# Performance work log

Hardware: AMD Instinct MI355X
Metric: run time of the kernel (lower is better)

## Reference

```python
import jax, jax.numpy as jnp
import numpy as np
from jax import lax

SEQ, BATCH, IN, HID, OUT = 168, 4096, 24, 64, 9


def _uniform(key, shape, scale):
    return jax.random.uniform(key, shape, jnp.float32, -scale, scale)


def setup_inputs() -> dict:
    key = jax.random.key(0)
    ks = jax.random.split(key, 12)
    s = 1.0 / np.sqrt(HID)  # PyTorch LSTM/Linear init scale
    return {
        "x": jax.random.normal(ks[0], (SEQ, BATCH, IN), jnp.float32),
        # layer 0 LSTM (PyTorch gate order: i, f, g, o stacked along dim 0)
        "W_ih0": _uniform(ks[1], (4 * HID, IN), s),
        "W_hh0": _uniform(ks[2], (4 * HID, HID), s),
        "b_ih0": _uniform(ks[3], (4 * HID,), s),
        "b_hh0": _uniform(ks[4], (4 * HID,), s),
        # layer 1 LSTM
        "W_ih1": _uniform(ks[5], (4 * HID, HID), s),
        "W_hh1": _uniform(ks[6], (4 * HID, HID), s),
        "b_ih1": _uniform(ks[7], (4 * HID,), s),
        "b_hh1": _uniform(ks[8], (4 * HID,), s),
        # linear head
        "W_out": _uniform(ks[9], (OUT, HID), s),
        "b_out": _uniform(ks[10], (OUT,), s),
    }


def _lstm_layer(x, W_ih, W_hh, b_ih, b_hh):
    # x: [S, B, D]; returns hidden states [S, B, H]
    H = W_hh.shape[1]
    B = x.shape[1]
    # precompute input projections for all timesteps: [S, B, 4H]
    xg = jnp.einsum('sbd,gd->sbg', x, W_ih) + b_ih + b_hh

    def step(carry, xg_t):
        h, c = carry
        g = xg_t + h @ W_hh.T  # [B, 4H]
        i, f, gc, o = jnp.split(g, 4, axis=-1)
        c = jax.nn.sigmoid(f) * c + jax.nn.sigmoid(i) * jnp.tanh(gc)
        h = jax.nn.sigmoid(o) * jnp.tanh(c)
        return (h, c), h

    init = (jnp.zeros((B, H), x.dtype), jnp.zeros((B, H), x.dtype))
    _, hs = lax.scan(step, init, xg)
    return hs


def reference(x, W_ih0, W_hh0, b_ih0, b_hh0, W_ih1, W_hh1, b_ih1, b_hh1, W_out, b_out):
    h = _lstm_layer(x, W_ih0, W_hh0, b_ih0, b_hh0)   # [S, B, H]
    h = _lstm_layer(h, W_ih1, W_hh1, b_ih1, b_hh1)   # [S, B, H]
    out = jnp.einsum('sbh,oh->sbo', h, W_out) + b_out  # [S, B, OUT]
    return out
```

## Files before the change

kernel.cpp:

```cpp
#include <hip/hip_runtime.h>
#include <hip/hip_bf16.h>
#include <math.h>

#define SEQ   168
#define BATCH 4096
#define NOUT  9
#define NBLK  256

typedef short bf16x8 __attribute__((ext_vector_type(8)));
typedef float f32x4  __attribute__((ext_vector_type(4)));

#define MFMA(a,b,c) __builtin_amdgcn_mfma_f32_16x16x32_bf16((a),(b),(c),0,0,0)

static __device__ __forceinline__ float bf2f(unsigned short h){
    unsigned int u = ((unsigned int)h) << 16;
    return __builtin_bit_cast(float, u);
}
static __device__ __forceinline__ unsigned short f2bf(float f){
    return __builtin_bit_cast(unsigned short, __float2bfloat16(f));
}
static __device__ __forceinline__ void splitf(float f, unsigned short& hi, unsigned short& lo){
    hi = f2bf(f);
    float r = f - bf2f(hi);
    lo = (unsigned short)(__builtin_bit_cast(unsigned int, r) >> 16);
}
static __device__ __forceinline__ float sigf(float x){
    return __builtin_amdgcn_rcpf(1.0f + __expf(-x));
}
static __device__ __forceinline__ float tanhf_(float x){
    float r = __builtin_amdgcn_rcpf(1.0f + __expf(2.0f * x));
    return fmaf(-2.0f, r, 1.0f);
}
static __device__ __forceinline__ bf16x8 ldfrag(const unsigned short* p){
    const uint4 q = *reinterpret_cast<const uint4*>(p);
    return __builtin_bit_cast(bf16x8, q);
}

static __device__ __forceinline__ void gbar(int* cnt, int* phs, int* done,
                                            int tickval, int& ph, int lane){
    asm volatile("s_waitcnt lgkmcnt(0)" ::: "memory");
    if (lane == 0){
        int old = __hip_atomic_fetch_add(cnt, 1, __ATOMIC_ACQ_REL,
                                         __HIP_MEMORY_SCOPE_WORKGROUP);
        if (old == 3){
            *cnt = 0;
            __hip_atomic_store(done, tickval, __ATOMIC_RELEASE,
                               __HIP_MEMORY_SCOPE_WORKGROUP);
            __hip_atomic_store(phs, ph ^ 1, __ATOMIC_RELEASE,
                               __HIP_MEMORY_SCOPE_WORKGROUP);
        }
    }
    while (__hip_atomic_load(phs, __ATOMIC_ACQUIRE,
                             __HIP_MEMORY_SCOPE_WORKGROUP) == ph)
        __builtin_amdgcn_s_sleep(1);
    ph ^= 1;
}
static __device__ __forceinline__ void wait_ge(int* done, int need){
    if (__hip_atomic_load(done, __ATOMIC_ACQUIRE, __HIP_MEMORY_SCOPE_WORKGROUP) >= need) return;
    do { __builtin_amdgcn_s_sleep(1); }
    while (__hip_atomic_load(done, __ATOMIC_ACQUIRE, __HIP_MEMORY_SCOPE_WORKGROUP) < need);
}

__global__ __launch_bounds__(512, 2)
void lstm_fused(const float* __restrict__ x,
                const float* __restrict__ Wih0, const float* __restrict__ Whh0,
                const float* __restrict__ bih0, const float* __restrict__ bhh0,
                const float* __restrict__ Wih1, const float* __restrict__ Whh1,
                const float* __restrict__ bih1, const float* __restrict__ bhh1,
                const float* __restrict__ Wout, const float* __restrict__ bout,
                float* __restrict__ out)
{
    __shared__ __align__(16) unsigned short sXH[2][16][72];
    __shared__ __align__(16) unsigned short sH0H[3][16][72];
    __shared__ __align__(16) unsigned short sH1H[2][16][72];
    __shared__ int sync[8];

    const int tid  = threadIdx.x;
    const int half = tid >> 8;
    const int w2   = (tid >> 6) & 3;
    const int l    = tid & 63;
    const int lr   = l & 15;
    const int g    = l >> 4;
    const int r0   = blockIdx.x * 16;
    const int cg   = w2 * 16 + lr;

    if (tid < 8) sync[tid] = (tid == 4) ? -1 : 0;

    for (int i = tid; i < (int)(2*16*72/2); i += 512){
        ((unsigned int*)sXH)[i]  = 0u;
        ((unsigned int*)sH1H)[i] = 0u;
    }
    for (int i = tid; i < (int)(3*16*72/2); i += 512)
        ((unsigned int*)sH0H)[i] = 0u;
    __syncthreads();
    if (tid < 96){
        const float4 v = *reinterpret_cast<const float4*>(&x[(size_t)r0 * 24 + tid * 4]);
        const int row = (tid * 4) / 24, col = (tid * 4) % 24;
        ushort4 w = { f2bf(v.x), f2bf(v.y), f2bf(v.z), f2bf(v.w) };
        *reinterpret_cast<ushort4*>(&sXH[0][row][col]) = w;
    }
    __syncthreads();

    if (half == 0){
        bf16x8 B0H[4][3];
        #pragma unroll
        for (int gt = 0; gt < 4; ++gt){
            const int c = gt * 64 + cg;
            bf16x8 bh = {0,0,0,0,0,0,0,0};
            if (g < 3){
                const float* pw = &Wih0[c * 24 + g * 8];
                #pragma unroll
                for (int j = 0; j < 8; ++j) bh[j] = (short)f2bf(pw[j]);
            }
            B0H[gt][0] = bh;
            #pragma unroll
            for (int ks = 0; ks < 2; ++ks){
                bf16x8 ch;
                const float* pw = &Whh0[c * 64 + ks * 32 + g * 8];
                #pragma unroll
                for (int j = 0; j < 8; ++j) ch[j] = (short)f2bf(pw[j]);
                B0H[gt][1+ks] = ch;
            }
        }
        float b0[4];
        #pragma unroll
        for (int gt = 0; gt < 4; ++gt) b0[gt] = bih0[gt*64 + cg] + bhh0[gt*64 + cg];

        const float* xfp = x + ((size_t)BATCH + r0) * 24 + tid * 4;
        float c0[4] = {0,0,0,0};
        int ph = 0;
        int pw = 0, pr = 2;
        for (int t = 0; t < SEQ; ++t){
            const int px = t & 1;
            const bool ldx = (tid < 96) && (t + 1 < SEQ);
            float4 pref;
            if (ldx){ pref = *reinterpret_cast<const float4*>(xfp); xfp += (size_t)BATCH * 24; }

            const bf16x8 AxH = ldfrag(&sXH[px][lr][g*8]);
            bf16x8 A0H[2];
            #pragma unroll
            for (int ks = 0; ks < 2; ++ks)
                A0H[ks] = ldfrag(&sH0H[pr][lr][ks*32 + g*8]);

            f32x4 a0[4];
            #pragma unroll
            for (int gt = 0; gt < 4; ++gt){ f32x4 a = {b0[gt],b0[gt],b0[gt],b0[gt]}; a0[gt] = a; }
            #pragma unroll
            for (int gt = 0; gt < 4; ++gt) a0[gt] = MFMA(AxH, B0H[gt][0], a0[gt]);
            #pragma unroll
            for (int ks = 0; ks < 2; ++ks){
                #pragma unroll
                for (int gt = 0; gt < 4; ++gt) a0[gt] = MFMA(A0H[ks], B0H[gt][1+ks], a0[gt]);
            }
            unsigned short hh[4];
            #pragma unroll
            for (int i = 0; i < 4; ++i){
                const float ig = sigf(a0[0][i]);
                const float fg = sigf(a0[1][i]);
                const float gg = tanhf_(a0[2][i]);
                const float og = sigf(a0[3][i]);
                c0[i] = fg * c0[i] + ig * gg;
                hh[i] = f2bf(og * tanhf_(c0[i]));
            }
            if (t >= 3) wait_ge(&sync[5], t - 2);
            #pragma unroll
            for (int i = 0; i < 4; ++i)
                sH0H[pw][g * 4 + i][cg] = hh[i];
            if (ldx){
                const int row = (tid * 4) / 24, col = (tid * 4) % 24;
                ushort4 w = { f2bf(pref.x), f2bf(pref.y), f2bf(pref.z), f2bf(pref.w) };
                *reinterpret_cast<ushort4*>(&sXH[px ^ 1][row][col]) = w;
            }
            gbar(&sync[0], &sync[2], &sync[4], t, ph, l);
            pr = pw;
            pw = (pw == 2) ? 0 : pw + 1;
        }
    } else {
        bf16x8 B1H[4][4];
        #pragma unroll
        for (int gt = 0; gt < 4; ++gt){
            const int c = gt * 64 + cg;
            #pragma unroll
            for (int ks = 0; ks < 2; ++ks){
                bf16x8 ch;
                const float* pw = &Wih1[c * 64 + ks * 32 + g * 8];
                #pragma unroll
                for (int j = 0; j < 8; ++j) ch[j] = (short)f2bf(pw[j]);
                B1H[gt][ks] = ch;
            }
            #pragma unroll
            for (int ks = 0; ks < 2; ++ks){
                bf16x8 ch;
                const float* pw = &Whh1[c * 64 + ks * 32 + g * 8];
                #pragma unroll
                for (int j = 0; j < 8; ++j) ch[j] = (short)f2bf(pw[j]);
                B1H[gt][2+ks] = ch;
            }
        }
        float b1[4];
        #pragma unroll
        for (int gt = 0; gt < 4; ++gt) b1[gt] = bih1[gt*64 + cg] + bhh1[gt*64 + cg];

        const int oc = lr;
        bf16x8 WoH[2], WoL[2];
        #pragma unroll
        for (int tt = 0; tt < 2; ++tt){
            bf16x8 bh = {0,0,0,0,0,0,0,0}, bl = {0,0,0,0,0,0,0,0};
            if (oc < NOUT){
                const float* pw = &Wout[oc * 64 + tt * 32 + g * 8];
                #pragma unroll
                for (int j = 0; j < 8; ++j){ unsigned short hh, ll; splitf(pw[j], hh, ll); bh[j]=(short)hh; bl[j]=(short)ll; }
            }
            WoH[tt] = bh; WoL[tt] = bl;
        }
        const float bo0 = (oc < NOUT) ? bout[oc] : 0.f;
        float* houtp = out + (size_t)(r0 + g * 4) * NOUT + oc;

        float c1[4] = {0,0,0,0};
        int ph = 0;
        int pr0 = 0;
        for (int t = 1; t <= SEQ; ++t){
            const int p = t & 1;
            bf16x8 A1H[2];
            #pragma unroll
            for (int ks = 0; ks < 2; ++ks)
                A1H[ks] = ldfrag(&sH1H[p][lr][ks*32 + g*8]);
            wait_ge(&sync[4], t - 1);
            bf16x8 A0H[2];
            #pragma unroll
            for (int ks = 0; ks < 2; ++ks)
                A0H[ks] = ldfrag(&sH0H[pr0][lr][ks*32 + g*8]);

            f32x4 a1[4];
            #pragma unroll
            for (int gt = 0; gt < 4; ++gt){ f32x4 a = {b1[gt],b1[gt],b1[gt],b1[gt]}; a1[gt] = a; }
            #pragma unroll
            for (int ks = 0; ks < 2; ++ks){
                #pragma unroll
                for (int gt = 0; gt < 4; ++gt) a1[gt] = MFMA(A1H[ks], B1H[gt][2+ks], a1[gt]);
            }
            if (t >= 2 && w2 == (t & 3)){
                f32x4 ha = {bo0, bo0, bo0, bo0};
                ha = MFMA(A1H[0], WoH[0], ha);
                ha = MFMA(A1H[0], WoL[0], ha);
                ha = MFMA(A1H[1], WoH[1], ha);
                ha = MFMA(A1H[1], WoL[1], ha);
                if (oc < NOUT){
                    #pragma unroll
                    for (int i = 0; i < 4; ++i)
                        houtp[(size_t)i * NOUT] = ha[i];
                }
            }
            if (t >= 2) houtp += (size_t)BATCH * NOUT;
            #pragma unroll
            for (int ks = 0; ks < 2; ++ks){
                #pragma unroll
                for (int gt = 0; gt < 4; ++gt) a1[gt] = MFMA(A0H[ks], B1H[gt][ks], a1[gt]);
            }
            #pragma unroll
            for (int i = 0; i < 4; ++i){
                const float ig = sigf(a1[0][i]);
                const float fg = sigf(a1[1][i]);
                const float gg = tanhf_(a1[2][i]);
                const float og = sigf(a1[3][i]);
                c1[i] = fg * c1[i] + ig * gg;
                sH1H[p ^ 1][g * 4 + i][cg] = f2bf(og * tanhf_(c1[i]));
            }
            gbar(&sync[1], &sync[3], &sync[5], t, ph, l);
            pr0 = (pr0 == 2) ? 0 : pr0 + 1;
        }
        {
            const int pe = (SEQ + 1) & 1;
            if (w2 == ((SEQ + 1) & 3)){
                bf16x8 A1H0 = ldfrag(&sH1H[pe][lr][g*8]);
                bf16x8 A1H1 = ldfrag(&sH1H[pe][lr][32 + g*8]);
                f32x4 ha = {bo0, bo0, bo0, bo0};
                ha = MFMA(A1H0, WoH[0], ha);
                ha = MFMA(A1H0, WoL[0], ha);
                ha = MFMA(A1H1, WoH[1], ha);
                ha = MFMA(A1H1, WoL[1], ha);
                if (oc < NOUT){
                    #pragma unroll
                    for (int i = 0; i < 4; ++i)
                        houtp[(size_t)i * NOUT] = ha[i];
                }
            }
        }
    }
}

extern "C" void kernel_launch(void* const* d_in, const int* in_sizes, int n_in,
                              void* d_out, int out_size, void* d_ws, size_t ws_size,
                              hipStream_t stream)
{
    const float* x    = (const float*)d_in[0];
    const float* Wih0 = (const float*)d_in[1];
    const float* Whh0 = (const float*)d_in[2];
    const float* bih0 = (const float*)d_in[3];
    const float* bhh0 = (const float*)d_in[4];
    const float* Wih1 = (const float*)d_in[5];
    const float* Whh1 = (const float*)d_in[6];
    const float* bih1 = (const float*)d_in[7];
    const float* bhh1 = (const float*)d_in[8];
    const float* Wout = (const float*)d_in[9];
    const float* bout = (const float*)d_in[10];
    float* out = (float*)d_out;

    lstm_fused<<<NBLK, 512, 0, stream>>>(x, Wih0, Whh0, bih0, bhh0,
                                         Wih1, Whh1, bih1, bhh1,
                                         Wout, bout, out);
}
```

Before: 166.2 us.

## Fold log2e scaling into LSTM weights and merge gate reciprocals

Pre-scales the gate weights and biases by log2(e), or 2*log2(e) for the tanh gate, so the activations can use exp2 directly. The cell update is rewritten so one reciprocal covers the i/f/g combination and one covers the output, replacing five separate reciprocals per element. Exponent arguments are clamped to avoid overflow. Separately, the s_sleep in the barrier spin loop is removed to cut wake-up latency, at the cost of more polling pressure on LDS.

```diff
diff --git a/kernel.cpp b/kernel.cpp
--- a/kernel.cpp
+++ b/kernel.cpp
@@ -12,6 +12,9 @@
 
 #define MFMA(a,b,c) __builtin_amdgcn_mfma_f32_16x16x32_bf16((a),(b),(c),0,0,0)
 
+#define L2E  1.44269504088896340736f
+#define CLMP 40.0f
+
 static __device__ __forceinline__ float bf2f(unsigned short h){
     unsigned int u = ((unsigned int)h) << 16;
     return __builtin_bit_cast(float, u);
@@ -24,16 +27,23 @@
     float r = f - bf2f(hi);
     lo = (unsigned short)(__builtin_bit_cast(unsigned int, r) >> 16);
 }
-static __device__ __forceinline__ float sigf(float x){
-    return __builtin_amdgcn_rcpf(1.0f + __expf(-x));
-}
-static __device__ __forceinline__ float tanhf_(float x){
-    float r = __builtin_amdgcn_rcpf(1.0f + __expf(2.0f * x));
-    return fmaf(-2.0f, r, 1.0f);
-}
 static __device__ __forceinline__ bf16x8 ldfrag(const unsigned short* p){
     const uint4 q = *reinterpret_cast<const uint4*>(p);
     return __builtin_bit_cast(bf16x8, q);
+}
+
+static __device__ __forceinline__ float cellupd(float pi, float pf, float pg,
+                                                float po, float& c){
+    const float Ai = 1.0f + exp2f(fminf(-pi, CLMP));
+    const float Af = 1.0f + exp2f(fminf(-pf, CLMP));
+    const float Bg = 1.0f + exp2f(fminf( pg, CLMP));
+    const float Ao = 1.0f + exp2f(fminf(-po, CLMP));
+    const float t1 = Ai * Bg;
+    const float r  = __builtin_amdgcn_rcpf(Af * t1);
+    const float cn = fmaf(c, t1, Af * (Bg - 2.0f)) * r;
+    c = cn;
+    const float Bc = 1.0f + exp2f(fminf(cn * (2.0f * L2E), CLMP));
+    return (Bc - 2.0f) * __builtin_amdgcn_rcpf(Ao * Bc);
 }
 
 static __device__ __forceinline__ void gbar(int* cnt, int* phs, int* done,
@@ -51,8 +61,7 @@
         }
     }
     while (__hip_atomic_load(phs, __ATOMIC_ACQUIRE,
-                             __HIP_MEMORY_SCOPE_WORKGROUP) == ph)
-        __builtin_amdgcn_s_sleep(1);
+                             __HIP_MEMORY_SCOPE_WORKGROUP) == ph) { }
     ph ^= 1;
 }
 static __device__ __forceinline__ void wait_ge(int* done, int need){
@@ -83,6 +92,8 @@
     const int g    = l >> 4;
     const int r0   = blockIdx.x * 16;
     const int cg   = w2 * 16 + lr;
+
+    const float WS[4] = { L2E, L2E, 2.0f * L2E, L2E };
 
     if (tid < 8) sync[tid] = (tid == 4) ? -1 : 0;
 
@@ -106,11 +117,12 @@
         #pragma unroll
         for (int gt = 0; gt < 4; ++gt){
             const int c = gt * 64 + cg;
+            const float sc = WS[gt];
             bf16x8 bh = {0,0,0,0,0,0,0,0};
             if (g < 3){
                 const float* pw = &Wih0[c * 24 + g * 8];
                 #pragma unroll
-                for (int j = 0; j < 8; ++j) bh[j] = (short)f2bf(pw[j]);
+                for (int j = 0; j < 8; ++j) bh[j] = (short)f2bf(pw[j] * sc);
             }
             B0H[gt][0] = bh;
             #pragma unroll
@@ -118,13 +130,13 @@
                 bf16x8 ch;
                 const float* pw = &Whh0[c * 64 + ks * 32 + g * 8];
                 #pragma unroll
-                for (int j = 0; j < 8; ++j) ch[j] = (short)f2bf(pw[j]);
+                for (int j = 0; j < 8; ++j) ch[j] = (short)f2bf(pw[j] * sc);
                 B0H[gt][1+ks] = ch;
             }
         }
         float b0[4];
         #pragma unroll
-        for (int gt = 0; gt < 4; ++gt) b0[gt] = bih0[gt*64 + cg] + bhh0[gt*64 + cg];
+        for (int gt = 0; gt < 4; ++gt) b0[gt] = (bih0[gt*64 + cg] + bhh0[gt*64 + cg]) * WS[gt];
 
         const float* xfp = x + ((size_t)BATCH + r0) * 24 + tid * 4;
         float c0[4] = {0,0,0,0};
@@ -154,14 +166,8 @@
             }
             unsigned short hh[4];
             #pragma unroll
-            for (int i = 0; i < 4; ++i){
-                const float ig = sigf(a0[0][i]);
-                const float fg = sigf(a0[1][i]);
-                const float gg = tanhf_(a0[2][i]);
-                const float og = sigf(a0[3][i]);
-                c0[i] = fg * c0[i] + ig * gg;
-                hh[i] = f2bf(og * tanhf_(c0[i]));
-            }
+            for (int i = 0; i < 4; ++i)
+                hh[i] = f2bf(cellupd(a0[0][i], a0[1][i], a0[2][i], a0[3][i], c0[i]));
             if (t >= 3) wait_ge(&sync[5], t - 2);
             #pragma unroll
             for (int i = 0; i < 4; ++i)
@@ -180,12 +186,13 @@
         #pragma unroll
         for (int gt = 0; gt < 4; ++gt){
             const int c = gt * 64 + cg;
+            const float sc = WS[gt];
             #pragma unroll
             for (int ks = 0; ks < 2; ++ks){
                 bf16x8 ch;
                 const float* pw = &Wih1[c * 64 + ks * 32 + g * 8];
                 #pragma unroll
-                for (int j = 0; j < 8; ++j) ch[j] = (short)f2bf(pw[j]);
+                for (int j = 0; j < 8; ++j) ch[j] = (short)f2bf(pw[j] * sc);
                 B1H[gt][ks] = ch;
             }
             #pragma unroll
@@ -193,13 +200,13 @@
                 bf16x8 ch;
                 const float* pw = &Whh1[c * 64 + ks * 32 + g * 8];
                 #pragma unroll
-                for (int j = 0; j < 8; ++j) ch[j] = (short)f2bf(pw[j]);
+                for (int j = 0; j < 8; ++j) ch[j] = (short)f2bf(pw[j] * sc);
                 B1H[gt][2+ks] = ch;
             }
         }
         float b1[4];
         #pragma unroll
-        for (int gt = 0; gt < 4; ++gt) b1[gt] = bih1[gt*64 + cg] + bhh1[gt*64 + cg];
+        for (int gt = 0; gt < 4; ++gt) b1[gt] = (bih1[gt*64 + cg] + bhh1[gt*64 + cg]) * WS[gt];
 
         const int oc = lr;
         bf16x8 WoH[2], WoL[2];
@@ -258,14 +265,9 @@
                 for (int gt = 0; gt < 4; ++gt) a1[gt] = MFMA(A0H[ks], B1H[gt][ks], a1[gt]);
             }
             #pragma unroll
-            for (int i = 0; i < 4; ++i){
-                const float ig = sigf(a1[0][i]);
-                const float fg = sigf(a1[1][i]);
-                const float gg = tanhf_(a1[2][i]);
-                const float og = sigf(a1[3][i]);
-                c1[i] = fg * c1[i] + ig * gg;
-                sH1H[p ^ 1][g * 4 + i][cg] = f2bf(og * tanhf_(c1[i]));
-            }
+            for (int i = 0; i < 4; ++i)
+                sH1H[p ^ 1][g * 4 + i][cg] =
+                    f2bf(cellupd(a1[0][i], a1[1][i], a1[2][i], a1[3][i], c1[i]));
             gbar(&sync[1], &sync[3], &sync[5], t, ph, l);
             pr0 = (pr0 == 2) ? 0 : pr0 + 1;
         }
```

After: 228.7 us. 1.38x slower.
